# Kernel tuning notes

Measured on AMD Instinct MI355X. Metric: run time of the kernel, lower is better.

## Reference

```python
import jax, jax.numpy as jnp
import numpy as np


def setup_inputs() -> dict:
    key = jax.random.key(0)
    k1, k2 = jax.random.split(key)
    n, c, h, w = 8, 2048, 64, 64
    out_c = 512
    fea = jax.random.normal(k1, (n, c, h, w), dtype=jnp.float32)
    # Conv2d weight [out, in, kh=1, kw=9]; kaiming-ish scale
    W = jax.random.normal(k2, (out_c, c, 1, 9), dtype=jnp.float32) * 0.02
    b = jnp.zeros((out_c,), dtype=jnp.float32)
    return {"fea": fea, "W": W, "b": b}


def reference(fea, W, b):
    # Original module (stride=1 path): for each width column i, take the
    # [n,c,h,1] slice, run Conv2d(kernel=(1,9), pad=(0,4)) + ReLU, concat on w.
    # For a width-1 input, only the CENTER kernel tap (kw index 4) overlaps
    # real data; all other taps see zero padding. Hence each column output is
    # ReLU(W[:,:,0,4] @ column + b), and the concat over columns is exactly a
    # pointwise (1x1) conv over the full feature map with the center tap.
    Wc = W[:, :, 0, 4]  # [out_c, in_c]
    out = jnp.einsum('nchw,oc->nohw', fea, Wc) + b[None, :, None, None]
    return jax.nn.relu(out)
```

## Files before the change

### kernel.cpp

```cpp
#include <hip/hip_runtime.h>
#include <hip/hip_bf16.h>

typedef __bf16 bf16x8 __attribute__((ext_vector_type(8)));
typedef float floatx4 __attribute__((ext_vector_type(4)));

#define KDIM 2048
#define MDIM 512
#define HWDIM 4096
#define BM 128
#define BN 128
#define BK 32

__device__ __forceinline__ void g2lds16(const void* g, void* l) {
  __builtin_amdgcn_global_load_lds(
      (const __attribute__((address_space(1))) unsigned int*)g,
      (__attribute__((address_space(3))) unsigned int*)l, 16, 0, 0);
}

__global__ void extract_w_kernel(const float* __restrict__ W, __bf16* __restrict__ Wc) {
  int idx = blockIdx.x * 256 + threadIdx.x;
  Wc[idx] = (__bf16)W[(size_t)idx * 9 + 4];
}

__global__ __launch_bounds__(256) void conv1x1_kernel(
    const float* __restrict__ fea, const __bf16* __restrict__ Wc,
    const float* __restrict__ bias, float* __restrict__ out) {
  __shared__ __align__(16) __bf16 As[BM * BK];
  __shared__ __align__(16) __bf16 Bs[BN * BK];

  const int t    = threadIdx.x;
  const int bx   = blockIdx.x;
  const int mb   = bx & 3;
  const int nb   = (bx >> 2) & 31;
  const int img  = bx >> 7;

  const int wave = t >> 6;
  const int lane = t & 63;
  const int l15  = lane & 15;
  const int quad = lane >> 4;
  const int wm   = (wave >> 1) * 64;
  const int wn   = (wave & 1) * 64;

  const float* feaN = fea + (size_t)img * ((size_t)KDIM * HWDIM) + nb * BN;
  float*       outN = out + (size_t)img * ((size_t)MDIM * HWDIM) + nb * BN;

  const int hw2 = t & 63;
  const int kg  = wave;
  const int r0  = 2 * hw2, r1 = r0 + 1;
  const int p0  = r0 ^ ((r0 >> 3) & 1);
  const int p1  = r1 ^ ((r1 >> 3) & 1);
  const int gsw = (kg ^ (hw2 & 3)) * 8;
  __bf16* bdst0 = &Bs[p0 * BK + gsw];
  __bf16* bdst1 = &Bs[p1 * BK + gsw];
  const float* bptr = feaN + (size_t)(kg * 8) * HWDIM + r0;

  const __bf16* gA0 = Wc + (size_t)(mb * BM + (t >> 2)) * KDIM + (t & 3) * 8;
  const __bf16* gA1 = gA0 + (size_t)64 * KDIM;
  __bf16* aDst0 = As + t * 8;
  __bf16* aDst1 = As + 2048 + t * 8;

  floatx4 acc[4][4];
#pragma unroll
  for (int i = 0; i < 4; ++i)
#pragma unroll
    for (int j = 0; j < 4; ++j) acc[i][j] = (floatx4){0.f, 0.f, 0.f, 0.f};

  for (int k0 = 0; k0 < KDIM; k0 += BK) {
    float2 v[8];
#pragma unroll
    for (int j = 0; j < 8; ++j) v[j] = *(const float2*)(bptr + (size_t)j * HWDIM);

    g2lds16(gA0 + k0, aDst0);
    g2lds16(gA1 + k0, aDst1);

    bf16x8 rowa, rowb;
#pragma unroll
    for (int j = 0; j < 8; ++j) { rowa[j] = (__bf16)v[j].x; rowb[j] = (__bf16)v[j].y; }
    *(bf16x8*)bdst0 = rowa;
    *(bf16x8*)bdst1 = rowb;

    __syncthreads();

    bf16x8 af[4], bf[4];
#pragma unroll
    for (int mt = 0; mt < 4; ++mt) {
      int m = wm + mt * 16 + l15;
      af[mt] = *(const bf16x8*)&As[m * BK + quad * 8];
    }
#pragma unroll
    for (int nt = 0; nt < 4; ++nt) {
      int n  = wn + nt * 16 + l15;
      int pn = n ^ ((n >> 3) & 1);
      int gq = quad ^ ((n >> 1) & 3);
      bf[nt] = *(const bf16x8*)&Bs[pn * BK + gq * 8];
    }
#pragma unroll
    for (int mt = 0; mt < 4; ++mt)
#pragma unroll
      for (int nt = 0; nt < 4; ++nt)
        acc[mt][nt] = __builtin_amdgcn_mfma_f32_16x16x32_bf16(af[mt], bf[nt], acc[mt][nt], 0, 0, 0);

    __syncthreads();
    bptr += (size_t)BK * HWDIM;
  }

#pragma unroll
  for (int mt = 0; mt < 4; ++mt) {
#pragma unroll
    for (int r = 0; r < 4; ++r) {
      int o = mb * BM + wm + mt * 16 + quad * 4 + r;
      float bv = bias[o];
      size_t rowoff = (size_t)o * HWDIM;
#pragma unroll
      for (int nt = 0; nt < 4; ++nt) {
        int hw = wn + nt * 16 + l15;
        float x = acc[mt][nt][r] + bv;
        outN[rowoff + hw] = x > 0.f ? x : 0.f;
      }
    }
  }
}

extern "C" void kernel_launch(void* const* d_in, const int* in_sizes, int n_in,
                              void* d_out, int out_size, void* d_ws, size_t ws_size,
                              hipStream_t stream) {
  const float* fea  = (const float*)d_in[0];
  const float* W    = (const float*)d_in[1];
  const float* bias = (const float*)d_in[2];
  float* out = (float*)d_out;
  __bf16* Wc = (__bf16*)d_ws;

  hipLaunchKernelGGL(extract_w_kernel, dim3(4096), dim3(256), 0, stream, W, Wc);
  hipLaunchKernelGGL(conv1x1_kernel, dim3(1024), dim3(256), 0, stream, fea, Wc, bias, out);
}
```

Before: 507.3 us.

## Cover all output channels per block and double-buffer the feature tile

Each block now covers all 512 output channels over a 64-wide spatial tile, using 8 waves, so every feature element is read from global memory exactly once instead of four times. Weights are loaded straight from global/L2 into registers rather than staged in LDS. The feature tile is double-buffered in LDS with next-iteration global loads overlapped with the MFMAs, and one barrier per iteration. The trade-off is per-lane scalar feature loads and uncached weight fetches each iteration, and only 512 blocks in the grid.

Result: faster. 495.4 us (-2.3%).

```diff
diff --git a/kernel.cpp b/kernel.cpp
--- a/kernel.cpp
+++ b/kernel.cpp
@@ -1,63 +1,49 @@
 #include <hip/hip_runtime.h>
 #include <hip/hip_bf16.h>
 
+typedef __bf16 bf16x4 __attribute__((ext_vector_type(4)));
 typedef __bf16 bf16x8 __attribute__((ext_vector_type(8)));
 typedef float floatx4 __attribute__((ext_vector_type(4)));
 
 #define KDIM 2048
 #define MDIM 512
 #define HWDIM 4096
-#define BM 128
-#define BN 128
+#define BN 64
 #define BK 32
+#define NITER (KDIM / BK)
 
-__device__ __forceinline__ void g2lds16(const void* g, void* l) {
-  __builtin_amdgcn_global_load_lds(
-      (const __attribute__((address_space(1))) unsigned int*)g,
-      (__attribute__((address_space(3))) unsigned int*)l, 16, 0, 0);
+__global__ void extract_w_kernel(const float* __restrict__ W, __bf16* __restrict__ Wc) {
+  int e = (blockIdx.x * 256 + threadIdx.x) * 4;
+  bf16x4 h;
+#pragma unroll
+  for (int j = 0; j < 4; ++j) h[j] = (__bf16)W[(size_t)(e + j) * 9 + 4];
+  *(bf16x4*)(Wc + e) = h;
 }
 
-__global__ void extract_w_kernel(const float* __restrict__ W, __bf16* __restrict__ Wc) {
-  int idx = blockIdx.x * 256 + threadIdx.x;
-  Wc[idx] = (__bf16)W[(size_t)idx * 9 + 4];
-}
-
-__global__ __launch_bounds__(256) void conv1x1_kernel(
+__global__ __launch_bounds__(512, 4) void conv1x1_kernel(
     const float* __restrict__ fea, const __bf16* __restrict__ Wc,
     const float* __restrict__ bias, float* __restrict__ out) {
-  __shared__ __align__(16) __bf16 As[BM * BK];
-  __shared__ __align__(16) __bf16 Bs[BN * BK];
+  __shared__ __align__(16) __bf16 Bs[2][BN * BK];
 
   const int t    = threadIdx.x;
-  const int bx   = blockIdx.x;
-  const int mb   = bx & 3;
-  const int nb   = (bx >> 2) & 31;
-  const int img  = bx >> 7;
-
   const int wave = t >> 6;
   const int lane = t & 63;
   const int l15  = lane & 15;
   const int quad = lane >> 4;
-  const int wm   = (wave >> 1) * 64;
-  const int wn   = (wave & 1) * 64;
+  const int wm   = wave * 64;
 
-  const float* feaN = fea + (size_t)img * ((size_t)KDIM * HWDIM) + nb * BN;
-  float*       outN = out + (size_t)img * ((size_t)MDIM * HWDIM) + nb * BN;
+  const int img = blockIdx.x >> 6;
+  const int nb  = blockIdx.x & 63;
 
-  const int hw2 = t & 63;
-  const int kg  = wave;
-  const int r0  = 2 * hw2, r1 = r0 + 1;
-  const int p0  = r0 ^ ((r0 >> 3) & 1);
-  const int p1  = r1 ^ ((r1 >> 3) & 1);
-  const int gsw = (kg ^ (hw2 & 3)) * 8;
-  __bf16* bdst0 = &Bs[p0 * BK + gsw];
-  __bf16* bdst1 = &Bs[p1 * BK + gsw];
-  const float* bptr = feaN + (size_t)(kg * 8) * HWDIM + r0;
+  const float* feaN = fea + (size_t)img * KDIM * HWDIM + (size_t)nb * BN;
+  float*       outN = out + (size_t)img * MDIM * HWDIM + (size_t)nb * BN;
 
-  const __bf16* gA0 = Wc + (size_t)(mb * BM + (t >> 2)) * KDIM + (t & 3) * 8;
-  const __bf16* gA1 = gA0 + (size_t)64 * KDIM;
-  __bf16* aDst0 = As + t * 8;
-  __bf16* aDst1 = As + 2048 + t * 8;
+  const int hw   = lane;
+  const int kg   = wave;
+  const int boff = hw * BK + (kg ^ ((hw >> 1) & 7)) * 4;
+  const float* bsrc = feaN + (size_t)kg * 4 * HWDIM + hw;
+
+  const __bf16* aptr = Wc + (size_t)(wm + l15) * KDIM + quad * 8;
 
   floatx4 acc[4][4];
 #pragma unroll
@@ -65,57 +51,72 @@
 #pragma unroll
     for (int j = 0; j < 4; ++j) acc[i][j] = (floatx4){0.f, 0.f, 0.f, 0.f};
 
-  for (int k0 = 0; k0 < KDIM; k0 += BK) {
-    float2 v[8];
+  {
+    float v[4];
 #pragma unroll
-    for (int j = 0; j < 8; ++j) v[j] = *(const float2*)(bptr + (size_t)j * HWDIM);
+    for (int j = 0; j < 4; ++j) v[j] = bsrc[(size_t)j * HWDIM];
+    bf16x4 h;
+#pragma unroll
+    for (int j = 0; j < 4; ++j) h[j] = (__bf16)v[j];
+    *(bf16x4*)&Bs[0][boff] = h;
+  }
+  __syncthreads();
 
-    g2lds16(gA0 + k0, aDst0);
-    g2lds16(gA1 + k0, aDst1);
+  for (int iter = 0; iter < NITER; ++iter) {
+    const int cur = iter & 1;
 
-    bf16x8 rowa, rowb;
+    float vn[4];
+    if (iter + 1 < NITER) {
+      const float* p = bsrc + (size_t)(iter + 1) * BK * HWDIM;
 #pragma unroll
-    for (int j = 0; j < 8; ++j) { rowa[j] = (__bf16)v[j].x; rowb[j] = (__bf16)v[j].y; }
-    *(bf16x8*)bdst0 = rowa;
-    *(bf16x8*)bdst1 = rowb;
+      for (int j = 0; j < 4; ++j) vn[j] = p[(size_t)j * HWDIM];
+    }
 
-    __syncthreads();
+    bf16x8 af[4];
+    const __bf16* ap = aptr + iter * BK;
+#pragma unroll
+    for (int mt = 0; mt < 4; ++mt)
+      af[mt] = *(const bf16x8*)(ap + (size_t)mt * 16 * KDIM);
 
-    bf16x8 af[4], bf[4];
-#pragma unroll
-    for (int mt = 0; mt < 4; ++mt) {
-      int m = wm + mt * 16 + l15;
-      af[mt] = *(const bf16x8*)&As[m * BK + quad * 8];
-    }
+    bf16x8 bfr[4];
 #pragma unroll
     for (int nt = 0; nt < 4; ++nt) {
-      int n  = wn + nt * 16 + l15;
-      int pn = n ^ ((n >> 3) & 1);
-      int gq = quad ^ ((n >> 1) & 3);
-      bf[nt] = *(const bf16x8*)&Bs[pn * BK + gq * 8];
+      const int n  = nt * 16 + l15;
+      const int sw = (n >> 1) & 7;
+      const __bf16* row = &Bs[cur][n * BK];
+      union { bf16x8 v8; bf16x4 v4[2]; } u;
+      u.v4[0] = *(const bf16x4*)(row + ((quad * 2) ^ sw) * 4);
+      u.v4[1] = *(const bf16x4*)(row + ((quad * 2 + 1) ^ sw) * 4);
+      bfr[nt] = u.v8;
     }
+
 #pragma unroll
     for (int mt = 0; mt < 4; ++mt)
 #pragma unroll
       for (int nt = 0; nt < 4; ++nt)
-        acc[mt][nt] = __builtin_amdgcn_mfma_f32_16x16x32_bf16(af[mt], bf[nt], acc[mt][nt], 0, 0, 0);
+        acc[mt][nt] = __builtin_amdgcn_mfma_f32_16x16x32_bf16(af[mt], bfr[nt], acc[mt][nt], 0, 0, 0);
 
+    if (iter + 1 < NITER) {
+      bf16x4 hn;
+#pragma unroll
+      for (int j = 0; j < 4; ++j) hn[j] = (__bf16)vn[j];
+      *(bf16x4*)&Bs[cur ^ 1][boff] = hn;
+    }
     __syncthreads();
-    bptr += (size_t)BK * HWDIM;
   }
 
 #pragma unroll
   for (int mt = 0; mt < 4; ++mt) {
+    const int o0 = wm + mt * 16 + quad * 4;
+    const float4 bv = *(const float4*)(bias + o0);
+    const float bvr[4] = {bv.x, bv.y, bv.z, bv.w};
 #pragma unroll
     for (int r = 0; r < 4; ++r) {
-      int o = mb * BM + wm + mt * 16 + quad * 4 + r;
-      float bv = bias[o];
-      size_t rowoff = (size_t)o * HWDIM;
+      const size_t ro = (size_t)(o0 + r) * HWDIM;
 #pragma unroll
       for (int nt = 0; nt < 4; ++nt) {
-        int hw = wn + nt * 16 + l15;
-        float x = acc[mt][nt][r] + bv;
-        outN[rowoff + hw] = x > 0.f ? x : 0.f;
+        float x = acc[mt][nt][r] + bvr[r];
+        outN[ro + nt * 16 + l15] = x > 0.f ? x : 0.f;
       }
     }
   }
@@ -130,6 +131,6 @@
   float* out = (float*)d_out;
   __bf16* Wc = (__bf16*)d_ws;
 
-  hipLaunchKernelGGL(extract_w_kernel, dim3(4096), dim3(256), 0, stream, W, Wc);
-  hipLaunchKernelGGL(conv1x1_kernel, dim3(1024), dim3(256), 0, stream, fea, Wc, bias, out);
+  hipLaunchKernelGGL(extract_w_kernel, dim3(1024), dim3(256), 0, stream, W, Wc);
+  hipLaunchKernelGGL(conv1x1_kernel, dim3(512), dim3(512), 0, stream, fea, Wc, bias, out);
 }
```
